# Optimization experiments

Hardware: AMD Instinct MI355X
Metric: run time of the kernel (lower is better)

Reference implementation:

```python
import jax, jax.numpy as jnp
import numpy as np

NPOINT = 2048
NSAMPLE = 32
BN_EPS = 1e-5


def fps(xyz_t, npoint):
    """Furthest point sampling. xyz_t: [B,N,3] -> idx [B,npoint] (starts at index 0)."""
    B, N, _ = xyz_t.shape

    def step(carry, _):
        dist, last = carry  # dist [B,N], last [B]
        centroid = jnp.take_along_axis(xyz_t, last[:, None, None], axis=1)  # [B,1,3]
        d = jnp.sum((xyz_t - centroid) ** 2, axis=-1)  # [B,N]
        dist = jnp.minimum(dist, d)
        nxt = jnp.argmax(dist, axis=1).astype(jnp.int32)
        return (dist, nxt), last

    init = (jnp.full((B, N), 1e10, xyz_t.dtype), jnp.zeros((B,), jnp.int32))
    _, idx = jax.lax.scan(step, init, None, length=npoint)  # [npoint,B]
    return jnp.transpose(idx)  # [B,npoint]


def knn(k, query_t, ref_t):
    """query_t [B,S,3], ref_t [B,N,3] -> k-nearest indices [B,S,k]."""
    d = (jnp.sum(query_t ** 2, -1)[:, :, None]
         + jnp.sum(ref_t ** 2, -1)[:, None, :]
         - 2.0 * jnp.einsum('bsc,bnc->bsn', query_t, ref_t))  # [B,S,N]
    _, idx = jax.lax.top_k(-d, k)
    return idx


def group(feat_t, idx):
    """feat_t [B,N,C], idx [B,S,K] -> [B,S,K,C] gathered neighbors."""
    return jax.vmap(lambda f, i: f[i])(feat_t, idx)


def setup_inputs():
    key = jax.random.key(0)
    ks = jax.random.split(key, 8)
    B, N, C, D = 8, 8192, 3, 3
    mlp = [32, 32, 64]
    inp = {
        'xyz': jax.random.normal(ks[0], (B, C, N), jnp.float32),
        'points': jax.random.normal(ks[1], (B, D, N), jnp.float32),
    }
    last = D + 3  # conv input channels = in_channel + 3
    for i, oc in enumerate(mlp):
        inp[f'w{i}'] = jax.random.normal(ks[2 + i], (oc, last), jnp.float32) * (1.0 / np.sqrt(last))
        inp[f'g{i}'] = jnp.ones((oc,), jnp.float32)
        inp[f'b{i}'] = jnp.zeros((oc,), jnp.float32)
        last = oc
    return inp


def reference(xyz, points, w0, g0, b0, w1, g1, b1, w2, g2, b2):
    xyz_t = jnp.transpose(xyz, (0, 2, 1))        # [B,N,3]
    points_t = jnp.transpose(points, (0, 2, 1))  # [B,N,D]

    fps_idx = fps(xyz_t, NPOINT)                             # [B,S]
    new_xyz_t = jax.vmap(lambda f, i: f[i])(xyz_t, fps_idx)  # [B,S,3]

    knn_idx = knn(NSAMPLE, new_xyz_t, xyz_t)                 # [B,S,K]
    grouped_xyz = group(xyz_t, knn_idx)                      # [B,S,K,3]
    pos_diff = grouped_xyz - new_xyz_t[:, :, None, :]        # [B,S,K,3]
    grouped_pts = group(points_t, knn_idx)                   # [B,S,K,D]

    x = jnp.concatenate([pos_diff, grouped_pts], axis=-1)    # [B,S,K,3+D]
    for w, g, b in ((w0, g0, b0), (w1, g1, b1), (w2, g2, b2)):
        x = jnp.einsum('oc,bskc->bsko', w, x)                # 1x1 conv, no bias
        mean = jnp.mean(x, axis=(0, 1, 2))                   # BatchNorm2d (training stats)
        var = jnp.var(x, axis=(0, 1, 2))
        x = jax.nn.relu(g * (x - mean) * jax.lax.rsqrt(var + BN_EPS) + b)

    new_points = jnp.max(x, axis=2)  # max over K neighbors -> [B,S,C']
    new_xyz = jnp.transpose(new_xyz_t, (0, 2, 1))      # [B,3,S]
    new_points = jnp.transpose(new_points, (0, 2, 1))  # [B,C',S]
    return (new_xyz, new_points, fps_idx)
```

## Files before the change

kernel.cpp:

```cpp
#include <hip/hip_runtime.h>
#include <hip/hip_bf16.h>
#include <math.h>


#define NB 8
#define NN 8192
#define NS 2048
#define NK 32

__global__ __launch_bounds__(256) void prep_kernel(const float* __restrict__ xyz,
                                                   const float* __restrict__ pts,
                                                   float4* __restrict__ xyz4,
                                                   float4* __restrict__ pts4) {
  int g = blockIdx.x * 256 + threadIdx.x;
  int b = g >> 13, n = g & 8191;
  const float* xb = xyz + b * 3 * NN;
  float x = xb[n], y = xb[NN + n], z = xb[2 * NN + n];
  xyz4[g] = make_float4(x, y, z, fmaf(x, x, fmaf(y, y, z * z)));
  const float* pb = pts + b * 3 * NN;
  pts4[g] = make_float4(pb[n], pb[NN + n], pb[2 * NN + n], 0.f);
}

template <int CTRL>
__device__ __forceinline__ float dpp_max(float v) {
  int o = __builtin_amdgcn_update_dpp(__float_as_int(v), __float_as_int(v),
                                      CTRL, 0xf, 0xf, false);
  return fmaxf(v, __int_as_float(o));
}

__global__ __launch_bounds__(256, 1) void fps_kernel(const float4* __restrict__ xyz4,
                                                     float* __restrict__ out_nxyz,
                                                     float* __restrict__ out_fps,
                                                     float4* __restrict__ nxyz4) {
  int b = blockIdx.x, tid = threadIdx.x;
  int lane = tid & 63, wid = tid >> 6;
  __shared__ unsigned long long wslot[2][4];
  const float4* xb = xyz4 + b * NN;

  float px[32], py[32], pz[32], dist[32];
#pragma unroll
  for (int j = 0; j < 32; ++j) {
    float4 t = xb[(tid << 5) + j];
    px[j] = t.x; py[j] = t.y; pz[j] = t.z;
    dist[j] = 1e10f;
  }
  float4 c0 = xb[0];
  float cx = c0.x, cy = c0.y, cz = c0.z;
  if (tid == 0) {
    nxyz4[b * NS] = c0;
    out_nxyz[b * 3 * NS] = c0.x;
    out_nxyz[b * 3 * NS + NS] = c0.y;
    out_nxyz[b * 3 * NS + 2 * NS] = c0.z;
    out_fps[b * NS] = 0.f;
  }

  for (int s = 1; s < NS; ++s) {
    float best = -1.0f;
    int bj = 0;
#pragma unroll
    for (int j = 0; j < 32; ++j) {
      float dx = __fsub_rn(px[j], cx);
      float dy = __fsub_rn(py[j], cy);
      float dz = __fsub_rn(pz[j], cz);
      float d = __fadd_rn(__fadd_rn(__fmul_rn(dx, dx), __fmul_rn(dy, dy)),
                          __fmul_rn(dz, dz));
      d = fminf(dist[j], d);
      dist[j] = d;
      bool gt = d > best;
      best = gt ? d : best;
      bj = gt ? j : bj;
    }

    float m = best;
    m = dpp_max<0x111>(m);
    m = dpp_max<0x112>(m);
    m = dpp_max<0x114>(m);
    m = dpp_max<0x118>(m);
    m = dpp_max<0x142>(m);
    m = dpp_max<0x143>(m);
    float wmax = __int_as_float(__builtin_amdgcn_readlane(__float_as_int(m), 63));

    unsigned long long bl = __ballot(best == wmax);
    int l0 = __ffsll((unsigned long long)bl) - 1;
    int gcand = (tid << 5) + bj;
    int gw = __builtin_amdgcn_readlane(gcand, l0);

    if (lane == 0)
      wslot[s & 1][wid] = (((unsigned long long)__float_as_uint(wmax)) << 32) |
                          (unsigned)(8191 - gw);
    __syncthreads();

    unsigned long long v0 = wslot[s & 1][0], v1 = wslot[s & 1][1];
    unsigned long long v2 = wslot[s & 1][2], v3 = wslot[s & 1][3];
    unsigned long long va = v0 > v1 ? v0 : v1;
    unsigned long long vb = v2 > v3 ? v2 : v3;
    unsigned long long vm = va > vb ? va : vb;
    int gid = 8191 - (int)(unsigned)(vm & 0xFFFFFFFFull);

    float4 c = xb[gid];
    cx = c.x; cy = c.y; cz = c.z;
    if (tid == 0) {
      nxyz4[b * NS + s] = c;
      out_nxyz[b * 3 * NS + s] = c.x;
      out_nxyz[b * 3 * NS + NS + s] = c.y;
      out_nxyz[b * 3 * NS + 2 * NS + s] = c.z;
      out_fps[b * NS + s] = (float)gid;
    }
  }
}

__device__ __forceinline__ void insert32(float (&a)[32], float f) {
#pragma unroll
  for (int i = 31; i >= 1; --i) a[i] = fminf(a[i], fmaxf(a[i - 1], f));
  a[0] = fminf(a[0], f);
}

__global__ __launch_bounds__(256) void knn_kernel(const float4* __restrict__ xyz4,
                                                  const float4* __restrict__ nxyz4,
                                                  int* __restrict__ knn) {
  __shared__ float lbuf[256][33];
  int b = blockIdx.x >> 5, tile = blockIdx.x & 31;
  int tid = threadIdx.x;
  int q = tid & 63, chunk = tid >> 6;
  float4 Q = nxyz4[b * NS + tile * 64 + q];
  float qq = Q.w;
  float mx = -2.f * Q.x, my = -2.f * Q.y, mz = -2.f * Q.z;
  float arr[32];
#pragma unroll
  for (int i = 0; i < 32; ++i) arr[i] = __uint_as_float(0x7f7fffffu);

  const float4* refs = xyz4 + b * NN + chunk * 2048;
  int rbase = chunk * 2048;
  for (int r = 0; r < 2048; ++r) {
    float4 R = refs[r];
    float d = fmaf(R.x, mx, fmaf(R.y, my, fmaf(R.z, mz, R.w + qq)));
    d = fmaxf(d, 0.f);
    float f = __uint_as_float((__float_as_uint(d) & 0xFFFFE000u) | (unsigned)(rbase + r));
    if (f < arr[31]) insert32(arr, f);
  }
#pragma unroll
  for (int i = 0; i < 32; ++i) lbuf[tid][i] = arr[i];
  __syncthreads();
  if (tid < 64) {
    for (int c = 1; c < 4; ++c)
      for (int i = 0; i < 32; ++i) {
        float f = lbuf[c * 64 + tid][i];
        if (f < arr[31]) insert32(arr, f);
      }
    int base = (b * NS + tile * 64 + tid) * NK;
#pragma unroll
    for (int i = 0; i < 32; ++i) knn[base + i] = (int)(__float_as_uint(arr[i]) & 0x1FFFu);
  }
}

template <int STAGE>
__global__ __launch_bounds__(256) void mlp_kernel(
    const float4* __restrict__ xyz4, const float4* __restrict__ pts4,
    const float4* __restrict__ nxyz4, const int* __restrict__ knn,
    const float* __restrict__ w0, const float* __restrict__ w1,
    const float* __restrict__ w2, const float* __restrict__ ab,
    float* __restrict__ partials, float* __restrict__ out_np) {
  constexpr int C = (STAGE == 2) ? 64 : 32;
  constexpr int SM = (STAGE == 3) ? 8 * 64 * 32 : 512;
  __shared__ float smem[SM];
  int blk = blockIdx.x;
  int b = blk >> 6, s0 = (blk & 63) * 32;
  int tid = threadIdx.x, sl = tid & 31, ksec = tid >> 5;
  int lane = tid & 63, wid = tid >> 6;
  int s = s0 + sl;
  float4 Q = nxyz4[b * NS + s];
  const float4* xb = xyz4 + b * NN;
  const float4* pb = pts4 + b * NN;
  const int* kb = knn + (b * NS + s) * NK + ksec * 4;

  float acc1[(STAGE == 3) ? 64 : C];
  float acc2[(STAGE == 3) ? 1 : C];
  if constexpr (STAGE == 3) {
#pragma unroll
    for (int o = 0; o < 64; ++o) acc1[o] = -3.4e38f;
  } else {
#pragma unroll
    for (int o = 0; o < C; ++o) { acc1[o] = 0.f; acc2[o] = 0.f; }
  }

  for (int kk = 0; kk < 4; ++kk) {
    int nid = kb[kk];
    float4 R = xb[nid];
    float4 P = pb[nid];
    float x0[6] = {R.x - Q.x, R.y - Q.y, R.z - Q.z, P.x, P.y, P.z};
    float h[32];
#pragma unroll
    for (int o = 0; o < 32; ++o) {
      float a = w0[o * 6] * x0[0];
#pragma unroll
      for (int c = 1; c < 6; ++c) a = fmaf(w0[o * 6 + c], x0[c], a);
      h[o] = a;
    }
    if constexpr (STAGE == 0) {
#pragma unroll
      for (int o = 0; o < 32; ++o) { acc1[o] += h[o]; acc2[o] = fmaf(h[o], h[o], acc2[o]); }
    } else {
#pragma unroll
      for (int o = 0; o < 32; ++o) h[o] = fmaxf(fmaf(h[o], ab[o], ab[64 + o]), 0.f);
      float h1[32];
#pragma unroll
      for (int o = 0; o < 32; ++o) {
        float a = 0.f;
#pragma unroll
        for (int i = 0; i < 32; ++i) a = fmaf(w1[o * 32 + i], h[i], a);
        h1[o] = a;
      }
      if constexpr (STAGE == 1) {
#pragma unroll
        for (int o = 0; o < 32; ++o) { acc1[o] += h1[o]; acc2[o] = fmaf(h1[o], h1[o], acc2[o]); }
      } else {
#pragma unroll
        for (int o = 0; o < 32; ++o) h1[o] = fmaxf(fmaf(h1[o], ab[128 + o], ab[192 + o]), 0.f);
#pragma unroll
        for (int o = 0; o < 64; ++o) {
          float a = 0.f;
#pragma unroll
          for (int i = 0; i < 32; ++i) a = fmaf(w2[o * 32 + i], h1[i], a);
          if constexpr (STAGE == 2) {
            acc1[o] += a;
            acc2[o] = fmaf(a, a, acc2[o]);
          } else {
            acc1[o] = fmaxf(acc1[o], fmaxf(fmaf(a, ab[256 + o], ab[320 + o]), 0.f));
          }
        }
      }
    }
  }

  if constexpr (STAGE < 3) {
#pragma unroll
    for (int o = 0; o < C; ++o) {
      float v1 = acc1[o], v2 = acc2[o];
#pragma unroll
      for (int d = 1; d < 64; d <<= 1) { v1 += __shfl_xor(v1, d); v2 += __shfl_xor(v2, d); }
      acc1[o] = v1; acc2[o] = v2;
    }
    if (lane == 0) {
#pragma unroll
      for (int o = 0; o < C; ++o) {
        smem[wid * 2 * C + o] = acc1[o];
        smem[wid * 2 * C + C + o] = acc2[o];
      }
    }
    __syncthreads();
    if (tid < 2 * C) {
      float v = smem[tid] + smem[2 * C + tid] + smem[4 * C + tid] + smem[6 * C + tid];
      partials[blk * 128 + tid] = v;
    }
  } else {
#pragma unroll
    for (int o = 0; o < 64; ++o) smem[ksec * 2048 + o * 32 + sl] = acc1[o];
    __syncthreads();
#pragma unroll
    for (int i = 0; i < 8; ++i) {
      int e = i * 256 + tid;
      int ch = e >> 5, ss = e & 31;
      float v = smem[ch * 32 + ss];
#pragma unroll
      for (int ks = 1; ks < 8; ++ks) v = fmaxf(v, smem[ks * 2048 + ch * 32 + ss]);
      out_np[b * 64 * NS + ch * NS + s0 + ss] = v;
    }
  }
}

__global__ __launch_bounds__(256) void finalize_kernel(const float* __restrict__ partials,
                                                       const float* __restrict__ g,
                                                       const float* __restrict__ bt,
                                                       float* __restrict__ ab, int C) {
  __shared__ float sm[256];
  int tid = threadIdx.x;
  int ch = tid & 127, half = tid >> 7;
  float acc = 0.f;
  if (ch < 2 * C) {
    const float* p = partials + half * 256 * 128 + ch;
    for (int i = 0; i < 256; ++i) acc += p[i * 128];
  }
  sm[half * 128 + ch] = acc;
  __syncthreads();
  if (tid < C) {
    float s1 = sm[tid] + sm[128 + tid];
    float s2 = sm[C + tid] + sm[128 + C + tid];
    const float ninv = 1.0f / 524288.0f;
    float mean = s1 * ninv;
    float var = s2 * ninv - mean * mean;
    float inv = 1.0f / sqrtf(var + 1e-5f);
    float a = g[tid] * inv;
    ab[tid] = a;
    ab[64 + tid] = bt[tid] - mean * a;
  }
}

extern "C" void kernel_launch(void* const* d_in, const int* in_sizes, int n_in,
                              void* d_out, int out_size, void* d_ws, size_t ws_size,
                              hipStream_t stream) {
  const float* xyz = (const float*)d_in[0];
  const float* pts = (const float*)d_in[1];
  const float* w0 = (const float*)d_in[2];
  const float* g0 = (const float*)d_in[3];
  const float* b0 = (const float*)d_in[4];
  const float* w1 = (const float*)d_in[5];
  const float* g1 = (const float*)d_in[6];
  const float* b1 = (const float*)d_in[7];
  const float* w2 = (const float*)d_in[8];
  const float* g2 = (const float*)d_in[9];
  const float* b2 = (const float*)d_in[10];
  float* out = (float*)d_out;
  float* ws = (float*)d_ws;

  float4* xyz4 = (float4*)ws;
  float4* pts4 = (float4*)(ws + 262144);
  float4* nxyz4 = (float4*)(ws + 524288);
  int* knn = (int*)(ws + 589824);
  float* partials = ws + 1114112;
  float* ab = ws + 1310720;
  float* out_np = out + 49152;
  float* out_fps = out + 1097728;

  prep_kernel<<<256, 256, 0, stream>>>(xyz, pts, xyz4, pts4);
  fps_kernel<<<NB, 256, 0, stream>>>(xyz4, out, out_fps, nxyz4);
  knn_kernel<<<256, 256, 0, stream>>>(xyz4, nxyz4, knn);

  mlp_kernel<0><<<512, 256, 0, stream>>>(xyz4, pts4, nxyz4, knn, w0, w1, w2, ab, partials, nullptr);
  finalize_kernel<<<1, 256, 0, stream>>>(partials, g0, b0, ab, 32);
  mlp_kernel<1><<<512, 256, 0, stream>>>(xyz4, pts4, nxyz4, knn, w0, w1, w2, ab, partials + 65536, nullptr);
  finalize_kernel<<<1, 256, 0, stream>>>(partials + 65536, g1, b1, ab + 128, 32);
  mlp_kernel<2><<<512, 256, 0, stream>>>(xyz4, pts4, nxyz4, knn, w0, w1, w2, ab, partials + 131072, nullptr);
  finalize_kernel<<<1, 256, 0, stream>>>(partials + 131072, g2, b2, ab + 256, 64);
  mlp_kernel<3><<<512, 256, 0, stream>>>(xyz4, pts4, nxyz4, knn, w0, w1, w2, ab, nullptr, out_np);
}
```

Baseline: 3.085 ms.

## Spread FPS over 512 threads with LDS-resident points; unroll KNN scan

The FPS kernel now runs 512 threads per batch instead of 256. Point coordinates are staged once into shared memory (96 KB) rather than held in registers, and each thread owns 16 strided points. The centroid is read from LDS instead of global memory, and its squared norm is recomputed. The KNN reference loop is unrolled by four to issue loads early. The trade is an LDS read every iteration plus a wider 8-wave reduction, in exchange for more parallelism on the serial FPS critical path.

```diff
diff --git a/kernel.cpp b/kernel.cpp
--- a/kernel.cpp
+++ b/kernel.cpp
@@ -28,22 +28,24 @@
   return fmaxf(v, __int_as_float(o));
 }
 
-__global__ __launch_bounds__(256, 1) void fps_kernel(const float4* __restrict__ xyz4,
+__global__ __launch_bounds__(512, 2) void fps_kernel(const float4* __restrict__ xyz4,
                                                      float* __restrict__ out_nxyz,
                                                      float* __restrict__ out_fps,
                                                      float4* __restrict__ nxyz4) {
+  __shared__ float lxyz[3 * NN];
+  __shared__ unsigned long long wslot[2][8];
   int b = blockIdx.x, tid = threadIdx.x;
   int lane = tid & 63, wid = tid >> 6;
-  __shared__ unsigned long long wslot[2][4];
   const float4* xb = xyz4 + b * NN;
 
-  float px[32], py[32], pz[32], dist[32];
-#pragma unroll
-  for (int j = 0; j < 32; ++j) {
-    float4 t = xb[(tid << 5) + j];
-    px[j] = t.x; py[j] = t.y; pz[j] = t.z;
-    dist[j] = 1e10f;
-  }
+  for (int i = tid; i < NN; i += 512) {
+    float4 t = xb[i];
+    lxyz[3 * i] = t.x; lxyz[3 * i + 1] = t.y; lxyz[3 * i + 2] = t.z;
+  }
+  float dist[16];
+#pragma unroll
+  for (int j = 0; j < 16; ++j) dist[j] = 1e10f;
+
   float4 c0 = xb[0];
   float cx = c0.x, cy = c0.y, cz = c0.z;
   if (tid == 0) {
@@ -53,15 +55,17 @@
     out_nxyz[b * 3 * NS + 2 * NS] = c0.z;
     out_fps[b * NS] = 0.f;
   }
+  __syncthreads();
 
   for (int s = 1; s < NS; ++s) {
     float best = -1.0f;
     int bj = 0;
 #pragma unroll
-    for (int j = 0; j < 32; ++j) {
-      float dx = __fsub_rn(px[j], cx);
-      float dy = __fsub_rn(py[j], cy);
-      float dz = __fsub_rn(pz[j], cz);
+    for (int j = 0; j < 16; ++j) {
+      int p3 = 3 * (j * 512 + tid);
+      float dx = __fsub_rn(lxyz[p3], cx);
+      float dy = __fsub_rn(lxyz[p3 + 1], cy);
+      float dz = __fsub_rn(lxyz[p3 + 2], cz);
       float d = __fadd_rn(__fadd_rn(__fmul_rn(dx, dx), __fmul_rn(dy, dy)),
                           __fmul_rn(dz, dz));
       d = fminf(dist[j], d);
@@ -81,8 +85,8 @@
     float wmax = __int_as_float(__builtin_amdgcn_readlane(__float_as_int(m), 63));
 
     unsigned long long bl = __ballot(best == wmax);
-    int l0 = __ffsll((unsigned long long)bl) - 1;
-    int gcand = (tid << 5) + bj;
+    int l0 = __ffsll(bl) - 1;
+    int gcand = bj * 512 + tid;
     int gw = __builtin_amdgcn_readlane(gcand, l0);
 
     if (lane == 0)
@@ -90,20 +94,21 @@
                           (unsigned)(8191 - gw);
     __syncthreads();
 
-    unsigned long long v0 = wslot[s & 1][0], v1 = wslot[s & 1][1];
-    unsigned long long v2 = wslot[s & 1][2], v3 = wslot[s & 1][3];
-    unsigned long long va = v0 > v1 ? v0 : v1;
-    unsigned long long vb = v2 > v3 ? v2 : v3;
-    unsigned long long vm = va > vb ? va : vb;
+    unsigned long long vm = wslot[s & 1][0];
+#pragma unroll
+    for (int k = 1; k < 8; ++k) {
+      unsigned long long o = wslot[s & 1][k];
+      vm = o > vm ? o : vm;
+    }
     int gid = 8191 - (int)(unsigned)(vm & 0xFFFFFFFFull);
 
-    float4 c = xb[gid];
-    cx = c.x; cy = c.y; cz = c.z;
+    cx = lxyz[3 * gid]; cy = lxyz[3 * gid + 1]; cz = lxyz[3 * gid + 2];
     if (tid == 0) {
-      nxyz4[b * NS + s] = c;
-      out_nxyz[b * 3 * NS + s] = c.x;
-      out_nxyz[b * 3 * NS + NS + s] = c.y;
-      out_nxyz[b * 3 * NS + 2 * NS + s] = c.z;
+      float w = fmaf(cx, cx, fmaf(cy, cy, cz * cz));
+      nxyz4[b * NS + s] = make_float4(cx, cy, cz, w);
+      out_nxyz[b * 3 * NS + s] = cx;
+      out_nxyz[b * 3 * NS + NS + s] = cy;
+      out_nxyz[b * 3 * NS + 2 * NS + s] = cz;
       out_fps[b * NS + s] = (float)gid;
     }
   }
@@ -131,12 +136,23 @@
 
   const float4* refs = xyz4 + b * NN + chunk * 2048;
   int rbase = chunk * 2048;
-  for (int r = 0; r < 2048; ++r) {
-    float4 R = refs[r];
-    float d = fmaf(R.x, mx, fmaf(R.y, my, fmaf(R.z, mz, R.w + qq)));
-    d = fmaxf(d, 0.f);
-    float f = __uint_as_float((__float_as_uint(d) & 0xFFFFE000u) | (unsigned)(rbase + r));
-    if (f < arr[31]) insert32(arr, f);
+  for (int r = 0; r < 2048; r += 4) {
+    float4 R0 = refs[r];
+    float4 R1 = refs[r + 1];
+    float4 R2 = refs[r + 2];
+    float4 R3 = refs[r + 3];
+    float d0 = fmaxf(fmaf(R0.x, mx, fmaf(R0.y, my, fmaf(R0.z, mz, R0.w + qq))), 0.f);
+    float d1 = fmaxf(fmaf(R1.x, mx, fmaf(R1.y, my, fmaf(R1.z, mz, R1.w + qq))), 0.f);
+    float d2 = fmaxf(fmaf(R2.x, mx, fmaf(R2.y, my, fmaf(R2.z, mz, R2.w + qq))), 0.f);
+    float d3 = fmaxf(fmaf(R3.x, mx, fmaf(R3.y, my, fmaf(R3.z, mz, R3.w + qq))), 0.f);
+    float f0 = __uint_as_float((__float_as_uint(d0) & 0xFFFFE000u) | (unsigned)(rbase + r));
+    float f1 = __uint_as_float((__float_as_uint(d1) & 0xFFFFE000u) | (unsigned)(rbase + r + 1));
+    float f2 = __uint_as_float((__float_as_uint(d2) & 0xFFFFE000u) | (unsigned)(rbase + r + 2));
+    float f3 = __uint_as_float((__float_as_uint(d3) & 0xFFFFE000u) | (unsigned)(rbase + r + 3));
+    if (f0 < arr[31]) insert32(arr, f0);
+    if (f1 < arr[31]) insert32(arr, f1);
+    if (f2 < arr[31]) insert32(arr, f2);
+    if (f3 < arr[31]) insert32(arr, f3);
   }
 #pragma unroll
   for (int i = 0; i < 32; ++i) lbuf[tid][i] = arr[i];
@@ -322,7 +338,7 @@
   float* out_fps = out + 1097728;
 
   prep_kernel<<<256, 256, 0, stream>>>(xyz, pts, xyz4, pts4);
-  fps_kernel<<<NB, 256, 0, stream>>>(xyz4, out, out_fps, nxyz4);
+  fps_kernel<<<NB, 512, 0, stream>>>(xyz4, out, out_fps, nxyz4);
   knn_kernel<<<256, 256, 0, stream>>>(xyz4, nxyz4, knn);
 
   mlp_kernel<0><<<512, 256, 0, stream>>>(xyz4, pts4, nxyz4, knn, w0, w1, w2, ab, partials, nullptr);
```

Measured after the change: 3.298 ms. 1.07x slower.
